# Kernel tuning notes

Measured on AMD Instinct MI355X. Metric: run time of the kernel, lower is better.

## Reference

```python
import jax, jax.numpy as jnp
import numpy as np

B, T, C = 2, 2048, 2048
H, HKV, D = 16, 4, 128
THETA = 10000.0
G = H // HKV  # kv groups


def _rope_tables(seq_len, dim, theta):
    inv_freq = 1.0 / theta ** (jnp.arange(0, dim, 2, dtype=jnp.float32) / dim)
    t = jnp.arange(seq_len, dtype=jnp.float32)
    freqs = jnp.outer(t, inv_freq)                 # [T, D/2]
    emb = jnp.concatenate([freqs, freqs], axis=-1)  # [T, D]
    return jnp.cos(emb)[None, None], jnp.sin(emb)[None, None]  # [1,1,T,D]


def _rotate_half(x):
    x1, x2 = jnp.split(x, 2, axis=-1)
    return jnp.concatenate([-x2, x1], axis=-1)


def setup_inputs() -> dict:
    key = jax.random.key(0)
    ks = jax.random.split(key, 6)
    x = jax.random.normal(ks[0], (B, T, C), dtype=jnp.float32)
    s = 0.02
    Wq = jax.random.normal(ks[1], (C, H * D), dtype=jnp.float32) * s
    Wk = jax.random.normal(ks[2], (C, HKV * D), dtype=jnp.float32) * s
    Wv = jax.random.normal(ks[3], (C, HKV * D), dtype=jnp.float32) * s
    Wo = jax.random.normal(ks[4], (H * D, C), dtype=jnp.float32) * s
    mask = jnp.tril(jnp.ones((T, T), dtype=jnp.int32))[None, None]  # causal [1,1,T,T]
    return {"x": x, "Wq": Wq, "Wk": Wk, "Wv": Wv, "Wo": Wo, "mask": mask}


def reference(x, Wq, Wk, Wv, Wo, mask):
    b, t, _ = x.shape
    q = (x @ Wq).reshape(b, t, H, D).transpose(0, 2, 1, 3)      # [B,H,T,D]
    k = (x @ Wk).reshape(b, t, HKV, D).transpose(0, 2, 1, 3)    # [B,HKV,T,D]
    v = (x @ Wv).reshape(b, t, HKV, D).transpose(0, 2, 1, 3)
    cos, sin = _rope_tables(t, D, THETA)
    q = q * cos + _rotate_half(q) * sin
    k = k * cos + _rotate_half(k) * sin
    # expand kv heads (repeat_interleave over head axis)
    k = jnp.repeat(k, G, axis=1)                                # [B,H,T,D]
    v = jnp.repeat(v, G, axis=1)
    attn = jnp.einsum('bhqd,bhkd->bhqk', q, k) / jnp.sqrt(jnp.float32(D))
    attn = jnp.where(mask == 0, jnp.float32(-jnp.inf), attn)
    attn = jax.nn.softmax(attn, axis=-1)
    out = jnp.einsum('bhqk,bhkd->bhqd', attn, v)                # [B,H,T,D]
    out = out.transpose(0, 2, 1, 3).reshape(b, t, H * D)
    return out @ Wo
```

## Files before the change

### kernel.cpp

```cpp
#include <hip/hip_runtime.h>
#include <math.h>

#define B_ 2
#define T_ 2048
#define C_ 2048
#define H_ 16
#define HKV_ 4
#define D_ 128
#define G_ (H_ / HKV_)
#define GK 2048
#define NT9 32

typedef float f32x4 __attribute__((ext_vector_type(4)));
typedef __bf16 bf16x8 __attribute__((ext_vector_type(8)));

static __device__ __forceinline__ f32x4 mfma16(bf16x8 a, bf16x8 b, f32x4 c) {
    return __builtin_amdgcn_mfma_f32_16x16x32_bf16(a, b, c, 0, 0, 0);
}

static __device__ __forceinline__ void gload16(const __bf16* g, __bf16* l) {
    __builtin_amdgcn_global_load_lds(
        (const __attribute__((address_space(1))) unsigned int*)g,
        (__attribute__((address_space(3))) unsigned int*)l,
        16, 0, 0);
}

#define WRAP9(x) ((x) < 9 ? (x) : (x) - 9)

#define STG(SRC, h, kk, slot) {                                                 \
    _Pragma("unroll")                                                           \
    for (int j_ = 0; j_ < 2; ++j_) {                                            \
        const int lr_ = (h) * 128 + wave * 16 + j_ * 8 + (lane >> 3);           \
        const int sc_ = ((lane & 7) ^ (lane >> 3)) << 3;                        \
        gload16(&(SRC)[(size_t)lr_ * GK + (kk) + sc_],                          \
                &sl[slot][(wave * 16 + j_ * 8) * 64]);                          \
    } }

#define GEMM8_MAIN(At, Bt)                                                      \
    __shared__ __bf16 sl[9][8192];                                              \
    const int tid = threadIdx.x;                                                \
    const int wave = tid >> 6, lane = tid & 63;                                 \
    const int a = lane & 15, bq = lane >> 4;                                    \
    const int wr = wave >> 2, wc = wave & 3;                                    \
    const int xl = (a & 7) << 3;                                                \
    const int brow = (wc & 1) * 64;                                             \
    f32x4 acc[8][4];                                                            \
    _Pragma("unroll")                                                           \
    for (int mi = 0; mi < 8; ++mi)                                              \
        _Pragma("unroll")                                                       \
        for (int ni = 0; ni < 4; ++ni) acc[mi][ni] = (f32x4){0.f,0.f,0.f,0.f};  \
            \
    STG(At, 0, 0, 0) STG(At, 1, 0, 1) STG(Bt, 0, 0, 2) STG(Bt, 1, 0, 3)        \
    STG(At, 0, 64, 4)                                                           \
    int s0 = 0;                                                                 \
    _Pragma("unroll 1")                                                         \
    for (int t = 0; t < NT9; ++t) {                                             \
        if (t == NT9 - 1) { asm volatile("s_waitcnt vmcnt(0)" ::: "memory"); }  \
        else              { asm volatile("s_waitcnt vmcnt(2)" ::: "memory"); }  \
        __builtin_amdgcn_sched_barrier(0);                                      \
        __builtin_amdgcn_s_barrier();                                           \
        __builtin_amdgcn_sched_barrier(0);                                      \
        const int sA = WRAP9(s0 + wr);                                          \
        const int sB = WRAP9(s0 + 2 + (wc >> 1));                               \
        bf16x8 bf_[4][2];                                                       \
        _Pragma("unroll")                                                       \
        for (int ni = 0; ni < 4; ++ni)                                          \
            _Pragma("unroll")                                                   \
            for (int ks = 0; ks < 2; ++ks)                                      \
                bf_[ni][ks] = *(const bf16x8*)&sl[sB][(brow + ni*16 + a)*64 +   \
                                                      ((ks*32 + bq*8) ^ xl)];   \
        _Pragma("unroll")                                                       \
        for (int p = 0; p < 4; ++p) {                                           \
            bf16x8 af_[2][2];                                                   \
            _Pragma("unroll")                                                   \
            for (int m = 0; m < 2; ++m)                                         \
                _Pragma("unroll")                                               \
                for (int ks = 0; ks < 2; ++ks)                                  \
                    af_[m][ks] = *(const bf16x8*)&sl[sA][((p*2 + m)*16 + a)*64 +\
                                                         ((ks*32 + bq*8) ^ xl)];\
            if (p == 0 && t + 1 < NT9) STG(At, 1, (t+1)*64, WRAP9(s0 + 5))      \
            if (p == 1 && t + 1 < NT9) STG(Bt, 0, (t+1)*64, WRAP9(s0 + 6))      \
            if (p == 2 && t + 1 < NT9) STG(Bt, 1, (t+1)*64, WRAP9(s0 + 7))      \
            if (p == 3 && t + 2 < NT9) STG(At, 0, (t+2)*64, WRAP9(s0 + 8))      \
            __builtin_amdgcn_s_setprio(1);                                      \
            _Pragma("unroll")                                                   \
            for (int m = 0; m < 2; ++m)                                         \
                _Pragma("unroll")                                               \
                for (int ni = 0; ni < 4; ++ni) {                                \
                    acc[p*2+m][ni] = mfma16(af_[m][0], bf_[ni][0], acc[p*2+m][ni]); \
                    acc[p*2+m][ni] = mfma16(af_[m][1], bf_[ni][1], acc[p*2+m][ni]); \
                }                                                               \
            __builtin_amdgcn_s_setprio(0);                                      \
            if (p < 3) { __builtin_amdgcn_s_barrier(); }                        \
        }                                                                       \
        s0 += 4; if (s0 >= 9) s0 -= 9;                                          \
    }

__global__ __launch_bounds__(512, 1)
void gemm_qkv8(const __bf16* __restrict__ xb,
               const __bf16* __restrict__ wqt,
               const __bf16* __restrict__ wkt,
               const __bf16* __restrict__ wvt,
               __bf16* __restrict__ qbuf,
               __bf16* __restrict__ kbuf,
               __bf16* __restrict__ vbuf)
{
    const int bid = blockIdx.x;
    const int swz = (bid & 7) * 24 + (bid >> 3);
    const int mti = swz / 12, nti = swz % 12;
    const int m0 = mti * 256, n0 = nti * 256;

    const __bf16* Btp; __bf16* outb; int NH, nloc;
    if (n0 < 2048)      { Btp = wqt + (size_t)n0 * GK;          outb = qbuf; NH = 16; nloc = n0; }
    else if (n0 < 2560) { Btp = wkt + (size_t)(n0 - 2048) * GK; outb = kbuf; NH = 4;  nloc = n0 - 2048; }
    else                { Btp = wvt + (size_t)(n0 - 2560) * GK; outb = vbuf; NH = 4;  nloc = n0 - 2560; }
    const __bf16* Atp = xb + (size_t)m0 * GK;

    GEMM8_MAIN(Atp, Btp)

    #pragma unroll
    for (int mi = 0; mi < 8; ++mi)
        #pragma unroll
        for (int ni = 0; ni < 4; ++ni) {
            const int col = nloc + wc * 64 + ni * 16 + a;
            const int head = col >> 7, d = col & 127;
            #pragma unroll
            for (int rr = 0; rr < 4; ++rr) {
                const int row = m0 + wr * 128 + mi * 16 + bq * 4 + rr;
                const int b = row >> 11, tt = row & (T_ - 1);
                outb[(((size_t)(b * NH + head)) * T_ + tt) * D_ + d] =
                    (__bf16)acc[mi][ni][rr];
            }
        }
}

__global__ __launch_bounds__(512, 1)
void gemm_out8(const __bf16* __restrict__ ab,
               const __bf16* __restrict__ wot,
               float* __restrict__ outp)
{
    const int bid = blockIdx.x;
    const int swz = (bid & 7) * 16 + (bid >> 3);
    const int mti = swz / 8, nti = swz % 8;
    const int m0 = mti * 256, n0 = nti * 256;
    const __bf16* Atp = ab + (size_t)m0 * GK;
    const __bf16* Btp = wot + (size_t)n0 * GK;

    GEMM8_MAIN(Atp, Btp)

    #pragma unroll
    for (int mi = 0; mi < 8; ++mi)
        #pragma unroll
        for (int ni = 0; ni < 4; ++ni) {
            const int col = n0 + wc * 64 + ni * 16 + a;
            #pragma unroll
            for (int rr = 0; rr < 4; ++rr) {
                const int row = m0 + wr * 128 + mi * 16 + bq * 4 + rr;
                outp[(size_t)row * C_ + col] = acc[mi][ni][rr];
            }
        }
}

__global__ __launch_bounds__(256)
void conv_f32_bf16(const float* __restrict__ src, __bf16* __restrict__ dst, int n8)
{
    const int i = blockIdx.x * blockDim.x + threadIdx.x;
    if (i >= n8) return;
    const float4 a = *(const float4*)&src[(size_t)i * 8];
    const float4 b = *(const float4*)&src[(size_t)i * 8 + 4];
    bf16x8 o;
    o[0] = (__bf16)a.x; o[1] = (__bf16)a.y; o[2] = (__bf16)a.z; o[3] = (__bf16)a.w;
    o[4] = (__bf16)b.x; o[5] = (__bf16)b.y; o[6] = (__bf16)b.z; o[7] = (__bf16)b.w;
    *(bf16x8*)&dst[(size_t)i * 8] = o;
}

__global__ __launch_bounds__(256)
void tconv(const float* __restrict__ src, __bf16* __restrict__ dst, int N)
{
    __shared__ __bf16 tl[32][34];
    const int tx = threadIdx.x;
    const int ty = threadIdx.y;
    const int k0 = blockIdx.x * 32;
    const int n0 = blockIdx.y * 32;

    #pragma unroll
    for (int i = 0; i < 4; ++i) {
        const int r = ty + i * 8;
        tl[r][tx] = (__bf16)src[(size_t)(k0 + r) * N + n0 + tx];
    }
    __syncthreads();
    #pragma unroll
    for (int i = 0; i < 4; ++i) {
        const int r = ty + i * 8;
        dst[(size_t)(n0 + r) * GK + k0 + tx] = tl[tx][r];
    }
}

__global__ void rope_bf16(__bf16* __restrict__ buf)
{
    const int idx = blockIdx.x * blockDim.x + threadIdx.x;
    const int jj  = idx & 31;
    const int row = idx >> 5;
    const int t   = row & (T_ - 1);
    const int d   = jj * 2;

    const float LOG_THETA = 9.210340371976184f;
    const float f1 = (float)t * __expf(-(float)d       * (LOG_THETA / 64.0f));
    const float f2 = (float)t * __expf(-(float)(d + 1) * (LOG_THETA / 64.0f));
    float s1, c1, s2, c2;
    __sincosf(f1, &s1, &c1);
    __sincosf(f2, &s2, &c2);

    __bf16* p = buf + (size_t)row * D_ + d;
    const float x1a = (float)p[0],  x1b = (float)p[1];
    const float x2a = (float)p[64], x2b = (float)p[65];
    p[0]  = (__bf16)(x1a * c1 - x2a * s1);
    p[1]  = (__bf16)(x1b * c2 - x2b * s2);
    p[64] = (__bf16)(x2a * c1 + x1a * s1);
    p[65] = (__bf16)(x2b * c2 + x1b * s2);
}

__global__ __launch_bounds__(256)
void transpose_v(const __bf16* __restrict__ vb, __bf16* __restrict__ vtb)
{
    __shared__ __bf16 tl[32][33];
    const int tx = threadIdx.x;
    const int ty = threadIdx.y;
    const int t0 = blockIdx.x * 32;
    const int d0 = blockIdx.y * 32;
    const int bh = blockIdx.z;

    const __bf16* src = vb + ((size_t)bh * T_ + t0) * D_ + d0;
    #pragma unroll
    for (int i = 0; i < 4; ++i) {
        const int r = ty + i * 8;
        tl[r][tx] = src[(size_t)r * D_ + tx];
    }
    __syncthreads();
    __bf16* dst = vtb + ((size_t)bh * D_ + d0) * T_ + t0;
    #pragma unroll
    for (int i = 0; i < 4; ++i) {
        const int dl = ty + i * 8;
        dst[(size_t)dl * T_ + tx] = tl[tx][dl];
    }
}

#define KS_STRIDE 136
#define VS_STRIDE 36
#define PS_STRIDE 76

__global__ __launch_bounds__(512)
void flash_attn_mfma(const __bf16* __restrict__ qb,
                     const __bf16* __restrict__ kb,
                     const __bf16* __restrict__ vtb,
                     __bf16* __restrict__ abuf)
{
    __shared__ __bf16 KsL[64 * KS_STRIDE];
    __shared__ __bf16 VsL[2 * 128 * VS_STRIDE];
    __shared__ __bf16 PsL[8 * 16 * PS_STRIDE];

    const int tid  = threadIdx.x;
    const int wave = tid >> 6;
    const int lane = tid & 63;
    const int a    = lane & 15;
    const int bq   = lane >> 4;

    const int pair = blockIdx.x;
    const int bh   = blockIdx.y;
    const int b    = bh >> 4;
    const int h    = bh & 15;
    const int kvh  = h >> 2;

    const __bf16* kg  = kb  + (size_t)(b * HKV_ + kvh) * T_ * D_;
    const __bf16* vtg = vtb + (size_t)(b * HKV_ + kvh) * D_ * T_;

    const float scale2 = 0.12750176129424902f;

    for (int half = 0; half < 2; ++half) {
        const int qti = half == 0 ? (15 - pair) : pair;
        const int qt0 = qti * 128;
        const int ntiles = 2 * qti + 2;
        const int qrow_lo = qt0 + wave * 16;

        const __bf16* qg = qb + ((size_t)(b * H_ + h) * T_ + qrow_lo) * D_;
        bf16x8 qf[4];
        #pragma unroll
        for (int ks = 0; ks < 4; ++ks)
            qf[ks] = *(const bf16x8*)&qg[(size_t)a * D_ + ks * 32 + bq * 8];

        f32x4 oacc[8];
        #pragma unroll
        for (int dt = 0; dt < 8; ++dt) oacc[dt] = (f32x4){0.f, 0.f, 0.f, 0.f};
        float m_r[4] = {-INFINITY, -INFINITY, -INFINITY, -INFINITY};
        float l_r[4] = {0.f, 0.f, 0.f, 0.f};

        bf16x8 kpre[2], vpre[2];
        #pragma unroll
        for (int it = 0; it < 2; ++it) {
            const int idx = it * 512 + tid;
            const int r = idx >> 4, c8 = (idx & 15) * 8;
            kpre[it] = *(const bf16x8*)&kg[(size_t)r * D_ + c8];
            const int bo = idx & 3, dd = (idx >> 2) & 127, ss2 = idx >> 9;
            vpre[it] = *(const bf16x8*)&vtg[(size_t)dd * T_ + ss2 * 32 + bo * 8];
        }
        __syncthreads();
        #pragma unroll
        for (int it = 0; it < 2; ++it) {
            const int idx = it * 512 + tid;
            const int r = idx >> 4, c8 = (idx & 15) * 8;
            *(bf16x8*)&KsL[r * KS_STRIDE + c8] = kpre[it];
            const int bo = idx & 3, dd = (idx >> 2) & 127, ss2 = idx >> 9;
            *(bf16x8*)&VsL[(ss2 * 128 + dd) * VS_STRIDE + bo * 8] = vpre[it];
        }
        __syncthreads();

        for (int kt = 0; kt < ntiles; ++kt) {
            const int k0 = kt * 64;
            if (kt + 1 < ntiles) {
                const int k0n = k0 + 64;
                #pragma unroll
                for (int it = 0; it < 2; ++it) {
                    const int idx = it * 512 + tid;
                    const int r = idx >> 4, c8 = (idx & 15) * 8;
                    kpre[it] = *(const bf16x8*)&kg[(size_t)(k0n + r) * D_ + c8];
                    const int bo = idx & 3, dd = (idx >> 2) & 127, ss2 = idx >> 9;
                    vpre[it] = *(const bf16x8*)&vtg[(size_t)dd * T_ + k0n + ss2 * 32 + bo * 8];
                }
            }

            if (k0 <= qrow_lo + 15) {
                f32x4 sacc[4];
                #pragma unroll
                for (int nt = 0; nt < 4; ++nt) {
                    sacc[nt] = (f32x4){0.f, 0.f, 0.f, 0.f};
                    #pragma unroll
                    for (int ks = 0; ks < 4; ++ks) {
                        bf16x8 kf = *(const bf16x8*)&KsL[(nt * 16 + a) * KS_STRIDE + ks * 32 + bq * 8];
                        sacc[nt] = mfma16(qf[ks], kf, sacc[nt]);
                    }
                }

                float p[4][4];
                float mrow[4] = {-INFINITY, -INFINITY, -INFINITY, -INFINITY};
                const bool needmask = (k0 + 63 > qrow_lo);
                #pragma unroll
                for (int nt = 0; nt < 4; ++nt) {
                    const int kc = k0 + nt * 16 + a;
                    #pragma unroll
                    for (int r = 0; r < 4; ++r) {
                        const int qrow = qrow_lo + bq * 4 + r;
                        float s = sacc[nt][r] * scale2;
                        if (needmask) s = (kc <= qrow) ? s : -INFINITY;
                        p[nt][r] = s;
                        mrow[r] = fmaxf(mrow[r], s);
                    }
                }
                #pragma unroll
                for (int off = 1; off < 16; off <<= 1)
                    #pragma unroll
                    for (int r = 0; r < 4; ++r)
                        mrow[r] = fmaxf(mrow[r], __shfl_xor(mrow[r], off));

                float corr[4], psum[4];
                #pragma unroll
                for (int r = 0; r < 4; ++r) {
                    const float mnew = fmaxf(m_r[r], mrow[r]);
                    corr[r] = exp2f(m_r[r] - mnew);
                    m_r[r] = mnew;
                    psum[r] = 0.f;
                    #pragma unroll
                    for (int nt = 0; nt < 4; ++nt) {
                        const float pe = exp2f(p[nt][r] - mnew);
                        p[nt][r] = pe;
                        psum[r] += pe;
                    }
                }
                #pragma unroll
                for (int off = 1; off < 16; off <<= 1)
                    #pragma unroll
                    for (int r = 0; r < 4; ++r)
                        psum[r] += __shfl_xor(psum[r], off);
                #pragma unroll
                for (int r = 0; r < 4; ++r) l_r[r] = l_r[r] * corr[r] + psum[r];

                #pragma unroll
                for (int dt = 0; dt < 8; ++dt)
                    #pragma unroll
                    for (int r = 0; r < 4; ++r) oacc[dt][r] *= corr[r];

                #pragma unroll
                for (int nt = 0; nt < 4; ++nt)
                    #pragma unroll
                    for (int r = 0; r < 4; ++r)
                        PsL[(wave * 16 + bq * 4 + r) * PS_STRIDE + nt * 16 + a] = (__bf16)p[nt][r];

                bf16x8 pf[2];
                #pragma unroll
                for (int ss = 0; ss < 2; ++ss)
                    pf[ss] = *(const bf16x8*)&PsL[(wave * 16 + a) * PS_STRIDE + ss * 32 + bq * 8];
                #pragma unroll
                for (int dt = 0; dt < 8; ++dt) {
                    #pragma unroll
                    for (int ss = 0; ss < 2; ++ss) {
                        bf16x8 vf = *(const bf16x8*)&VsL[(ss * 128 + dt * 16 + a) * VS_STRIDE + bq * 8];
                        oacc[dt] = mfma16(pf[ss], vf, oacc[dt]);
                    }
                }
            }

            __syncthreads();
            if (kt + 1 < ntiles) {
                #pragma unroll
                for (int it = 0; it < 2; ++it) {
                    const int idx = it * 512 + tid;
                    const int r = idx >> 4, c8 = (idx & 15) * 8;
                    *(bf16x8*)&KsL[r * KS_STRIDE + c8] = kpre[it];
                    const int bo = idx & 3, dd = (idx >> 2) & 127, ss2 = idx >> 9;
                    *(bf16x8*)&VsL[(ss2 * 128 + dd) * VS_STRIDE + bo * 8] = vpre[it];
                }
                __syncthreads();
            }
        }

        float invl[4];
        #pragma unroll
        for (int r = 0; r < 4; ++r) invl[r] = 1.f / l_r[r];
        #pragma unroll
        for (int dt = 0; dt < 8; ++dt)
            #pragma unroll
            for (int r = 0; r < 4; ++r) {
                const int qrow = qrow_lo + bq * 4 + r;
                abuf[((size_t)(b * T_) + qrow) * (H_ * D_) + h * D_ + dt * 16 + a] =
                    (__bf16)(oacc[dt][r] * invl[r]);
            }
    }
}

extern "C" void kernel_launch(void* const* d_in, const int* in_sizes, int n_in,
                              void* d_out, int out_size, void* d_ws, size_t ws_size,
                              hipStream_t stream)
{
    (void)in_sizes; (void)n_in; (void)out_size; (void)ws_size;
    const float* x  = (const float*)d_in[0];
    const float* Wq = (const float*)d_in[1];
    const float* Wk = (const float*)d_in[2];
    const float* Wv = (const float*)d_in[3];
    const float* Wo = (const float*)d_in[4];
    float* out = (float*)d_out;

    __bf16* xb  = (__bf16*)d_ws;
    __bf16* wqt = xb  + (size_t)4096 * 2048;
    __bf16* wkt = wqt + (size_t)2048 * 2048;
    __bf16* wvt = wkt + (size_t)512 * 2048;
    __bf16* wot = wvt + (size_t)512 * 2048;
    __bf16* qb  = wot + (size_t)2048 * 2048;
    __bf16* kb  = qb  + (size_t)B_ * H_   * T_ * D_;
    __bf16* vb  = kb  + (size_t)B_ * HKV_ * T_ * D_;
    __bf16* vtb = vb  + (size_t)B_ * HKV_ * T_ * D_;
    __bf16* ab  = vtb + (size_t)B_ * HKV_ * T_ * D_;

    hipLaunchKernelGGL(conv_f32_bf16, dim3(4096), dim3(256), 0, stream,
                       x, xb, (int)((size_t)B_ * T_ * C_ / 8));
    hipLaunchKernelGGL(tconv, dim3(64, 64), dim3(32, 8), 0, stream, Wq, wqt, 2048);
    hipLaunchKernelGGL(tconv, dim3(64, 16), dim3(32, 8), 0, stream, Wk, wkt, 512);
    hipLaunchKernelGGL(tconv, dim3(64, 16), dim3(32, 8), 0, stream, Wv, wvt, 512);
    hipLaunchKernelGGL(tconv, dim3(64, 64), dim3(32, 8), 0, stream, Wo, wot, 2048);

    hipLaunchKernelGGL(gemm_qkv8, dim3(192), dim3(512), 0, stream,
                       xb, wqt, wkt, wvt, qb, kb, vb);

    hipLaunchKernelGGL(rope_bf16, dim3(B_ * (H_ + HKV_) * T_ * 32 / 256), dim3(256),
                       0, stream, qb);

    hipLaunchKernelGGL(transpose_v, dim3(T_ / 32, D_ / 32, B_ * HKV_), dim3(32, 8), 0, stream,
                       vb, vtb);

    hipLaunchKernelGGL(flash_attn_mfma, dim3(8, B_ * H_), dim3(512), 0, stream,
                       qb, kb, vtb, ab);

    hipLaunchKernelGGL(gemm_out8, dim3(128), dim3(512), 0, stream,
                       ab, wot, out);
}
```

Before: 355.7 us.

## Double attention KV tile to 128 keys with per-wave diagonal skipping and lazy rescale

The flash attention kernel now processes 128-key K/V tiles instead of 64, which halves the number of tile iterations and block barriers per query tile. On the diagonal tile each wave only computes the 16-key subtiles it needs, and unused P entries are zero-filled. It also adds a deferred max-rescale that keeps the running max when the new row max is within a bound of it, which skips the output-accumulator correction. The cost is more LDS and registers per block (lower occupancy) and bf16 P values that can reach up to 2^11 when the rescale is deferred.

```diff
diff --git a/kernel.cpp b/kernel.cpp
--- a/kernel.cpp
+++ b/kernel.cpp
@@ -49,7 +49,6 @@
     for (int mi = 0; mi < 8; ++mi)                                              \
         _Pragma("unroll")                                                       \
         for (int ni = 0; ni < 4; ++ni) acc[mi][ni] = (f32x4){0.f,0.f,0.f,0.f};  \
-            \
     STG(At, 0, 0, 0) STG(At, 1, 0, 1) STG(Bt, 0, 0, 2) STG(Bt, 1, 0, 3)        \
     STG(At, 0, 64, 4)                                                           \
     int s0 = 0;                                                                 \
@@ -247,7 +246,7 @@
 
 #define KS_STRIDE 136
 #define VS_STRIDE 36
-#define PS_STRIDE 76
+#define PS_STRIDE 136
 
 __global__ __launch_bounds__(512)
 void flash_attn_mfma(const __bf16* __restrict__ qb,
@@ -255,8 +254,8 @@
                      const __bf16* __restrict__ vtb,
                      __bf16* __restrict__ abuf)
 {
-    __shared__ __bf16 KsL[64 * KS_STRIDE];
-    __shared__ __bf16 VsL[2 * 128 * VS_STRIDE];
+    __shared__ __bf16 KsL[128 * KS_STRIDE];
+    __shared__ __bf16 VsL[4 * 128 * VS_STRIDE];
     __shared__ __bf16 PsL[8 * 16 * PS_STRIDE];
 
     const int tid  = threadIdx.x;
@@ -279,7 +278,7 @@
     for (int half = 0; half < 2; ++half) {
         const int qti = half == 0 ? (15 - pair) : pair;
         const int qt0 = qti * 128;
-        const int ntiles = 2 * qti + 2;
+        const int ntiles = qti + 1;
         const int qrow_lo = qt0 + wave * 16;
 
         const __bf16* qg = qb + ((size_t)(b * H_ + h) * T_ + qrow_lo) * D_;
@@ -294,9 +293,9 @@
         float m_r[4] = {-INFINITY, -INFINITY, -INFINITY, -INFINITY};
         float l_r[4] = {0.f, 0.f, 0.f, 0.f};
 
-        bf16x8 kpre[2], vpre[2];
-        #pragma unroll
-        for (int it = 0; it < 2; ++it) {
+        bf16x8 kpre[4], vpre[4];
+        #pragma unroll
+        for (int it = 0; it < 4; ++it) {
             const int idx = it * 512 + tid;
             const int r = idx >> 4, c8 = (idx & 15) * 8;
             kpre[it] = *(const bf16x8*)&kg[(size_t)r * D_ + c8];
@@ -305,7 +304,7 @@
         }
         __syncthreads();
         #pragma unroll
-        for (int it = 0; it < 2; ++it) {
+        for (int it = 0; it < 4; ++it) {
             const int idx = it * 512 + tid;
             const int r = idx >> 4, c8 = (idx & 15) * 8;
             *(bf16x8*)&KsL[r * KS_STRIDE + c8] = kpre[it];
@@ -315,11 +314,11 @@
         __syncthreads();
 
         for (int kt = 0; kt < ntiles; ++kt) {
-            const int k0 = kt * 64;
+            const int k0 = kt * 128;
             if (kt + 1 < ntiles) {
-                const int k0n = k0 + 64;
-                #pragma unroll
-                for (int it = 0; it < 2; ++it) {
+                const int k0n = k0 + 128;
+                #pragma unroll
+                for (int it = 0; it < 4; ++it) {
                     const int idx = it * 512 + tid;
                     const int r = idx >> 4, c8 = (idx & 15) * 8;
                     kpre[it] = *(const bf16x8*)&kg[(size_t)(k0n + r) * D_ + c8];
@@ -328,90 +327,108 @@
                 }
             }
 
-            if (k0 <= qrow_lo + 15) {
-                f32x4 sacc[4];
-                #pragma unroll
-                for (int nt = 0; nt < 4; ++nt) {
-                    sacc[nt] = (f32x4){0.f, 0.f, 0.f, 0.f};
+            const bool diag = (kt == ntiles - 1);
+            const int nlim  = diag ? wave : 7;
+            const int sslim = diag ? (wave >> 1) : 3;
+
+            float p[8][4];
+            float mrow[4] = {-INFINITY, -INFINITY, -INFINITY, -INFINITY};
+            #pragma unroll
+            for (int nt = 0; nt < 8; ++nt) {
+                if (nt <= nlim) {
+                    f32x4 sacc = (f32x4){0.f, 0.f, 0.f, 0.f};
                     #pragma unroll
                     for (int ks = 0; ks < 4; ++ks) {
                         bf16x8 kf = *(const bf16x8*)&KsL[(nt * 16 + a) * KS_STRIDE + ks * 32 + bq * 8];
-                        sacc[nt] = mfma16(qf[ks], kf, sacc[nt]);
+                        sacc = mfma16(qf[ks], kf, sacc);
                     }
-                }
-
-                float p[4][4];
-                float mrow[4] = {-INFINITY, -INFINITY, -INFINITY, -INFINITY};
-                const bool needmask = (k0 + 63 > qrow_lo);
-                #pragma unroll
-                for (int nt = 0; nt < 4; ++nt) {
                     const int kc = k0 + nt * 16 + a;
                     #pragma unroll
                     for (int r = 0; r < 4; ++r) {
-                        const int qrow = qrow_lo + bq * 4 + r;
-                        float s = sacc[nt][r] * scale2;
-                        if (needmask) s = (kc <= qrow) ? s : -INFINITY;
+                        float s = sacc[r] * scale2;
+                        if (diag) {
+                            const int qrow = qrow_lo + bq * 4 + r;
+                            s = (kc <= qrow) ? s : -INFINITY;
+                        }
                         p[nt][r] = s;
                         mrow[r] = fmaxf(mrow[r], s);
                     }
+                } else {
+                    #pragma unroll
+                    for (int r = 0; r < 4; ++r) p[nt][r] = -INFINITY;
                 }
-                #pragma unroll
-                for (int off = 1; off < 16; off <<= 1)
+            }
+            #pragma unroll
+            for (int off = 1; off < 16; off <<= 1)
+                #pragma unroll
+                for (int r = 0; r < 4; ++r)
+                    mrow[r] = fmaxf(mrow[r], __shfl_xor(mrow[r], off));
+
+            bool dfr = true;
+            #pragma unroll
+            for (int r = 0; r < 4; ++r) dfr = dfr && (mrow[r] <= m_r[r] + 11.0f);
+            dfr = __all(dfr);
+            float mnew[4];
+            #pragma unroll
+            for (int r = 0; r < 4; ++r)
+                mnew[r] = dfr ? m_r[r] : fmaxf(m_r[r], mrow[r]);
+
+            float psum[4] = {0.f, 0.f, 0.f, 0.f};
+            #pragma unroll
+            for (int nt = 0; nt < 8; ++nt) {
+                if (nt <= nlim) {
+                    #pragma unroll
+                    for (int r = 0; r < 4; ++r) {
+                        const float pe = exp2f(p[nt][r] - mnew[r]);
+                        psum[r] += pe;
+                        PsL[(wave * 16 + bq * 4 + r) * PS_STRIDE + nt * 16 + a] = (__bf16)pe;
+                    }
+                } else {
                     #pragma unroll
                     for (int r = 0; r < 4; ++r)
-                        mrow[r] = fmaxf(mrow[r], __shfl_xor(mrow[r], off));
-
-                float corr[4], psum[4];
+                        PsL[(wave * 16 + bq * 4 + r) * PS_STRIDE + nt * 16 + a] = (__bf16)0.f;
+                }
+            }
+            #pragma unroll
+            for (int off = 1; off < 16; off <<= 1)
+                #pragma unroll
+                for (int r = 0; r < 4; ++r)
+                    psum[r] += __shfl_xor(psum[r], off);
+
+            if (!dfr) {
+                float corr[4];
                 #pragma unroll
                 for (int r = 0; r < 4; ++r) {
-                    const float mnew = fmaxf(m_r[r], mrow[r]);
-                    corr[r] = exp2f(m_r[r] - mnew);
-                    m_r[r] = mnew;
-                    psum[r] = 0.f;
-                    #pragma unroll
-                    for (int nt = 0; nt < 4; ++nt) {
-                        const float pe = exp2f(p[nt][r] - mnew);
-                        p[nt][r] = pe;
-                        psum[r] += pe;
+                    corr[r] = exp2f(m_r[r] - mnew[r]);
+                    m_r[r] = mnew[r];
+                    l_r[r] = l_r[r] * corr[r] + psum[r];
+                }
+                #pragma unroll
+                for (int dt = 0; dt < 8; ++dt)
+                    #pragma unroll
+                    for (int r = 0; r < 4; ++r) oacc[dt][r] *= corr[r];
+            } else {
+                #pragma unroll
+                for (int r = 0; r < 4; ++r) l_r[r] += psum[r];
+            }
+
+            #pragma unroll
+            for (int ss = 0; ss < 4; ++ss) {
+                if (ss <= sslim) {
+                    const bf16x8 pf =
+                        *(const bf16x8*)&PsL[(wave * 16 + a) * PS_STRIDE + ss * 32 + bq * 8];
+                    #pragma unroll
+                    for (int dt = 0; dt < 8; ++dt) {
+                        bf16x8 vf = *(const bf16x8*)&VsL[(ss * 128 + dt * 16 + a) * VS_STRIDE + bq * 8];
+                        oacc[dt] = mfma16(pf, vf, oacc[dt]);
                     }
                 }
-                #pragma unroll
-                for (int off = 1; off < 16; off <<= 1)
-                    #pragma unroll
-                    for (int r = 0; r < 4; ++r)
-                        psum[r] += __shfl_xor(psum[r], off);
-                #pragma unroll
-                for (int r = 0; r < 4; ++r) l_r[r] = l_r[r] * corr[r] + psum[r];
-
-                #pragma unroll
-                for (int dt = 0; dt < 8; ++dt)
-                    #pragma unroll
-                    for (int r = 0; r < 4; ++r) oacc[dt][r] *= corr[r];
-
-                #pragma unroll
-                for (int nt = 0; nt < 4; ++nt)
-                    #pragma unroll
-                    for (int r = 0; r < 4; ++r)
-                        PsL[(wave * 16 + bq * 4 + r) * PS_STRIDE + nt * 16 + a] = (__bf16)p[nt][r];
-
-                bf16x8 pf[2];
-                #pragma unroll
-                for (int ss = 0; ss < 2; ++ss)
-                    pf[ss] = *(const bf16x8*)&PsL[(wave * 16 + a) * PS_STRIDE + ss * 32 + bq * 8];
-                #pragma unroll
-                for (int dt = 0; dt < 8; ++dt) {
-                    #pragma unroll
-                    for (int ss = 0; ss < 2; ++ss) {
-                        bf16x8 vf = *(const bf16x8*)&VsL[(ss * 128 + dt * 16 + a) * VS_STRIDE + bq * 8];
-                        oacc[dt] = mfma16(pf[ss], vf, oacc[dt]);
-                    }
-                }
             }
 
             __syncthreads();
             if (kt + 1 < ntiles) {
                 #pragma unroll
-                for (int it = 0; it < 2; ++it) {
+                for (int it = 0; it < 4; ++it) {
                     const int idx = it * 512 + tid;
                     const int r = idx >> 4, c8 = (idx & 15) * 8;
                     *(bf16x8*)&KsL[r * KS_STRIDE + c8] = kpre[it];
```

Result: faster. 344.1 us (-3.3%).
